# Kernel tuning notes

Measured on AMD Instinct MI355X. Metric: run time of the kernel, lower is better.

The kernel has to match this reference:

```python
import jax, jax.numpy as jnp
import numpy as np

ALPHA = jnp.full((8,), 0.25, dtype=jnp.float32)  # per-class focal alpha
GAMMA = 2.0
TEMP = 0.07
CIRC_TARGET = 1.0
CIRC_WEIGHT = 0.1
MIN_AGREE = 0.6
W_FOCAL, W_CONTRAST, W_CONSENSUS = 1.0, 0.5, 0.3


def setup_inputs() -> dict:
    key = jax.random.key(0)
    k1, k2, k3, k4, k5 = jax.random.split(key, 5)
    return {
        "logits": jax.random.normal(k1, (32, 8, 256, 256), dtype=jnp.float32),
        "target": jax.random.randint(k2, (32, 256, 256), 0, 8, dtype=jnp.int32),
        "features": jax.random.normal(k3, (1024, 512), dtype=jnp.float32),
        "masks": jax.random.uniform(k4, (32, 3, 256, 256), dtype=jnp.float32),
        "method_preds": jax.random.uniform(k5, (3, 32, 256, 256), dtype=jnp.float32),
    }


def focal_loss(logits, target):
    B, C, H, W = logits.shape
    x = logits.transpose(0, 2, 3, 1).reshape(-1, C)  # [BHW, C]
    t = target.reshape(-1)
    logp = jax.nn.log_softmax(x, axis=-1)
    ce = -jnp.take_along_axis(logp, t[:, None], axis=1)[:, 0]
    p = jnp.exp(-ce)
    focal_w = ALPHA[t] * (1.0 - p) ** GAMMA
    return jnp.mean(focal_w * ce)


def contrastive_loss(features):
    Bf = features.shape[0]
    f = features / jnp.linalg.norm(features, axis=1, keepdims=True)
    sim = (f @ f.T) / TEMP  # [Bf, Bf]
    # default labels = arange(Bf//2) tiled twice -> each sample has exactly one
    # positive: its paired view at index (i + Bf//2) % Bf
    pos_idx = (jnp.arange(Bf) + Bf // 2) % Bf
    pos = sim[jnp.arange(Bf), pos_idx]
    diag = jnp.eye(Bf, dtype=bool)
    # logits row i = {positive_i} U negatives_i = all j != i (single positive case)
    masked = jnp.where(diag, -1e30, sim)
    lse = jax.nn.logsumexp(masked, axis=1)
    return jnp.mean(lse - pos)  # CE with target = the (only) positive


def circularity_loss(masks):
    m = masks[:, 0]  # [B, H, W] core channel
    B = m.shape[0]
    area = jnp.sum(m, axis=(1, 2))
    ex = jnp.sum(jnp.abs(m[:, 1:, :] - m[:, :-1, :]), axis=(1, 2))
    ey = jnp.sum(jnp.abs(m[:, :, 1:] - m[:, :, :-1]), axis=(1, 2))
    per = ex + ey
    circ = 4.0 * np.pi * area / jnp.maximum(per, 1e-12) ** 2
    li = jnp.where((area > 0) & (per > 0), (circ - CIRC_TARGET) ** 2, 0.0)
    return CIRC_WEIGHT * jnp.sum(li) / B


def consensus_loss(method_preds):
    K = method_preds.shape[0]
    total, n = 0.0, 0
    for i in range(K):  # K=3 methods -> 3 pairs (fixed, small)
        for j in range(i + 1, K):
            pi, pj = method_preds[i], method_preds[j]
            inter = jnp.sum(pi * pj)
            union = jnp.sum(pi + pj - pi * pj)
            iou = inter / (union + 1e-6)
            total = total + jax.nn.relu(MIN_AGREE - iou)
            n += 1
    return total / n


def reference(logits, target, features, masks, method_preds):
    return (W_FOCAL * focal_loss(logits, target)
            + W_CONTRAST * contrastive_loss(features)
            + circularity_loss(masks)
            + W_CONSENSUS * consensus_loss(method_preds))
```

## Files before the change

kernel.cpp:

```cpp
#include <hip/hip_runtime.h>
#include <math.h>

#define WS_FOCALP 0
#define WS_CONSP  2048
#define WS_AREAP  14336
#define WS_EXP_   14848
#define WS_EYP_   15360
#define WS_POS    15872
#define WS_PART   16896
#define WS_HI_B   393216
#define WS_LO_B   1441792

typedef __attribute__((ext_vector_type(8))) short bf16x8;
typedef __attribute__((ext_vector_type(4))) float f32x4;

__device__ inline float wave_reduce(float v) {
#pragma unroll
  for (int m = 32; m >= 1; m >>= 1) v += __shfl_xor(v, m);
  return v;
}

__device__ inline unsigned short bf16_rne(float x) {
  union { float f; unsigned u; } v; v.f = x;
  unsigned r = v.u + 0x7FFF + ((v.u >> 16) & 1);
  return (unsigned short)(r >> 16);
}
__device__ inline float bf16_f(unsigned short h) {
  union { unsigned u; float f; } v; v.u = ((unsigned)h) << 16; return v.f;
}

__device__ inline float focal_px(float v0, float v1, float v2, float v3,
                                 float v4, float v5, float v6, float v7, int tt) {
  float mx = fmaxf(fmaxf(fmaxf(v0, v1), fmaxf(v2, v3)),
                   fmaxf(fmaxf(v4, v5), fmaxf(v6, v7)));
  float se = __expf(v0 - mx) + __expf(v1 - mx) + __expf(v2 - mx) + __expf(v3 - mx) +
             __expf(v4 - mx) + __expf(v5 - mx) + __expf(v6 - mx) + __expf(v7 - mx);
  float xt = v0;
  xt = (tt == 1) ? v1 : xt;
  xt = (tt == 2) ? v2 : xt;
  xt = (tt == 3) ? v3 : xt;
  xt = (tt == 4) ? v4 : xt;
  xt = (tt == 5) ? v5 : xt;
  xt = (tt == 6) ? v6 : xt;
  xt = (tt == 7) ? v7 : xt;
  float lp = (xt - mx) - __logf(se);
  float p = __expf(lp);
  float om = 1.0f - p;
  return 0.25f * om * om * (-lp);
}

__global__ __launch_bounds__(256) void prep_kernel(const float* __restrict__ feat,
                                                   float* __restrict__ ws) {
  const int tid = threadIdx.x;
  const int lane = tid & 63;
  const int wid = tid >> 6;
  int row = blockIdx.x * 4 + wid;
  const float4* f4 = (const float4*)feat;
  float4 u = f4[row * 128 + lane];
  float4 w = f4[row * 128 + 64 + lane];
  float s = u.x * u.x + u.y * u.y + u.z * u.z + u.w * u.w +
            w.x * w.x + w.y * w.y + w.z * w.z + w.w * w.w;
  s = wave_reduce(s);
  float scale = 3.7796447300922719f / sqrtf(s);
  float g[8] = {u.x * scale, u.y * scale, u.z * scale, u.w * scale,
                w.x * scale, w.y * scale, w.z * scale, w.w * scale};
  unsigned short h[8];
  unsigned short l[8];
#pragma unroll
  for (int i = 0; i < 8; i++) {
    h[i] = bf16_rne(g[i]);
    l[i] = bf16_rne(g[i] - bf16_f(h[i]));
  }
  char* hb = (char*)ws + WS_HI_B + row * 1024;
  char* lb = (char*)ws + WS_LO_B + row * 1024;
  *(ushort4*)(hb + lane * 8) = make_ushort4(h[0], h[1], h[2], h[3]);
  *(ushort4*)(hb + 512 + lane * 8) = make_ushort4(h[4], h[5], h[6], h[7]);
  *(ushort4*)(lb + lane * 8) = make_ushort4(l[0], l[1], l[2], l[3]);
  *(ushort4*)(lb + 512 + lane * 8) = make_ushort4(l[4], l[5], l[6], l[7]);
}

__global__ __launch_bounds__(256) void fused_kernel(
    const float* __restrict__ logits, const int* __restrict__ target,
    const float* __restrict__ masks, const float* __restrict__ preds,
    float* __restrict__ ws) {
  __shared__ __align__(16) char lds[49152];
  const int bid = blockIdx.x;
  const int tid = threadIdx.x;
  const int lane = tid & 63;
  const int wid = tid >> 6;

  if (bid < 512) {
    const int wr = wid >> 1, wc = wid & 1;
    const int rt = bid >> 4, ct = bid & 15;
    const int rb = rt * 32, cb = ct * 64;
    const int hi8 = lane >> 4;
    const int l15 = lane & 15;
    const int lr_a = wr * 16 + l15;
    const int rb0 = wc * 32 + l15;
    const int rb1 = rb0 + 16;

    f32x4 acc0 = {0.f, 0.f, 0.f, 0.f};
    f32x4 acc1 = {0.f, 0.f, 0.f, 0.f};

    auto stage = [&](int ch) {
      const char* srcA = (const char*)ws + (ch < 8 ? WS_HI_B : WS_LO_B);
      const char* srcB = (const char*)ws + ((ch >> 2) == 1 ? WS_LO_B : WS_HI_B);
      int koff = (ch & 3) * 256;
      char* dst = lds + (ch & 1) * 24576;
#pragma unroll
      for (int rr = 0; rr < 6; rr++) {
        int idx = rr * 256 + tid;
        const char* g;
        if (rr < 2) {
          int row = idx >> 4, sl = idx & 15;
          g = srcA + (rb + row) * 1024 + koff + ((sl ^ (row & 7)) << 4);
        } else {
          int i2 = idx - 512;
          int row = i2 >> 4, sl = i2 & 15;
          g = srcB + (cb + row) * 1024 + koff + ((sl ^ (row & 7)) << 4);
        }
        __builtin_amdgcn_global_load_lds(
            (const __attribute__((address_space(1))) unsigned int*)g,
            (__attribute__((address_space(3))) unsigned int*)(dst + idx * 16),
            16, 0, 0);
      }
    };

    auto compute = [&](int buf) {
      const char* bp = lds + buf * 24576;
#pragma unroll
      for (int j = 0; j < 4; j++) {
        int sa = (j * 4 + hi8) ^ (lr_a & 7);
        bf16x8 a = *(const bf16x8*)(bp + lr_a * 256 + sa * 16);
        int sb0 = (j * 4 + hi8) ^ (rb0 & 7);
        bf16x8 b0 = *(const bf16x8*)(bp + 8192 + rb0 * 256 + sb0 * 16);
        int sb1 = (j * 4 + hi8) ^ (rb1 & 7);
        bf16x8 b1 = *(const bf16x8*)(bp + 8192 + rb1 * 256 + sb1 * 16);
        acc0 = __builtin_amdgcn_mfma_f32_16x16x32_bf16(a, b0, acc0, 0, 0, 0);
        acc1 = __builtin_amdgcn_mfma_f32_16x16x32_bf16(a, b1, acc1, 0, 0, 0);
      }
    };

    stage(0);
    __syncthreads();
#pragma unroll 1
    for (int ch = 0; ch < 12; ch++) {
      if (ch + 1 < 12) stage(ch + 1);
      compute(ch & 1);
      __syncthreads();
    }

    int c0 = cb + wc * 32 + l15;
    int c1 = c0 + 16;
    float2* part = (float2*)(ws + WS_PART);
#pragma unroll
    for (int q = 0; q < 4; q++) {
      int r = rb + wr * 16 + hi8 * 4 + q;
      float v0 = acc0[q], v1 = acc1[q];
      int pc = (r + 512) & 1023;
      if (c0 == pc) ws[WS_POS + r] = v0;
      if (c1 == pc) ws[WS_POS + r] = v1;
      if (c0 == r) v0 = -1e30f;
      if (c1 == r) v1 = -1e30f;
      float m = fmaxf(v0, v1);
      float s = __expf(v0 - m) + __expf(v1 - m);
#pragma unroll
      for (int d = 1; d < 16; d <<= 1) {
        float mo = __shfl_xor(m, d), so = __shfl_xor(s, d);
        float nm = fmaxf(m, mo);
        s = s * __expf(m - nm) + so * __expf(mo - nm);
        m = nm;
      }
      if (l15 == 0) part[r * 32 + ct * 2 + wc] = make_float2(m, s);
    }
    return;
  }

  float* red = (float*)lds;
  const int bid2 = bid - 512;

  if (bid2 < 2048) {
    int t = bid2 * 256 + tid;
    int p4 = t * 4;
    int b = p4 >> 16;
    int hw = p4 & 65535;
    const float* lb = logits + (b << 19) + hw;
    float4 x0 = *(const float4*)(lb + (0 << 16));
    float4 x1 = *(const float4*)(lb + (1 << 16));
    float4 x2 = *(const float4*)(lb + (2 << 16));
    float4 x3 = *(const float4*)(lb + (3 << 16));
    float4 x4 = *(const float4*)(lb + (4 << 16));
    float4 x5 = *(const float4*)(lb + (5 << 16));
    float4 x6 = *(const float4*)(lb + (6 << 16));
    float4 x7 = *(const float4*)(lb + (7 << 16));
    int4 tg = *(const int4*)(target + p4);
    float acc = 0.0f;
    acc += focal_px(x0.x, x1.x, x2.x, x3.x, x4.x, x5.x, x6.x, x7.x, tg.x);
    acc += focal_px(x0.y, x1.y, x2.y, x3.y, x4.y, x5.y, x6.y, x7.y, tg.y);
    acc += focal_px(x0.z, x1.z, x2.z, x3.z, x4.z, x5.z, x6.z, x7.z, tg.z);
    acc += focal_px(x0.w, x1.w, x2.w, x3.w, x4.w, x5.w, x6.w, x7.w, tg.w);
    float v = wave_reduce(acc);
    if (lane == 0) red[wid] = v;
    __syncthreads();
    if (tid == 0) ws[WS_FOCALP + bid2] = red[0] + red[1] + red[2] + red[3];

  } else if (bid2 < 2560) {
    int bi = bid2 - 2048;
    int img = bi >> 4;
    int part = bi & 15;
    const float* mS = masks + img * 3 * 65536;
    const float4* m4 = (const float4*)mS;
    float a = 0.0f, ex = 0.0f, ey = 0.0f;
#pragma unroll
    for (int i = 0; i < 4; i++) {
      int v = tid + 256 * i;
      int rl = v >> 6;
      int c4 = v & 63;
      int row = part * 16 + rl;
      float4 val = m4[row * 64 + c4];
      a += val.x + val.y + val.z + val.w;
      ey += fabsf(val.y - val.x) + fabsf(val.z - val.y) + fabsf(val.w - val.z);
      if (c4 > 0) ey += fabsf(val.x - mS[row * 256 + c4 * 4 - 1]);
      if (row > 0) {
        float4 u = m4[(row - 1) * 64 + c4];
        ex += fabsf(val.x - u.x) + fabsf(val.y - u.y) +
              fabsf(val.z - u.z) + fabsf(val.w - u.w);
      }
    }
    float ra = wave_reduce(a);
    float rx = wave_reduce(ex);
    float ry = wave_reduce(ey);
    if (lane == 0) {
      red[wid + 0] = ra; red[wid + 4] = rx; red[wid + 8] = ry;
    }
    __syncthreads();
    if (tid == 0) {
      ws[WS_AREAP + bi] = red[0] + red[1] + red[2] + red[3];
      ws[WS_EXP_ + bi] = red[4] + red[5] + red[6] + red[7];
      ws[WS_EYP_ + bi] = red[8] + red[9] + red[10] + red[11];
    }

  } else {
    int b = bid2 - 2560;
    int t = b * 256 + tid;
    const float4* q = (const float4*)preds;
    float4 a0 = q[t];
    float4 a1 = q[t + 524288];
    float4 a2 = q[t + 1048576];
    float s0 = a0.x + a0.y + a0.z + a0.w;
    float s1 = a1.x + a1.y + a1.z + a1.w;
    float s2 = a2.x + a2.y + a2.z + a2.w;
    float p01 = a0.x * a1.x + a0.y * a1.y + a0.z * a1.z + a0.w * a1.w;
    float p02 = a0.x * a2.x + a0.y * a2.y + a0.z * a2.z + a0.w * a2.w;
    float p12 = a1.x * a2.x + a1.y * a2.y + a1.z * a2.z + a1.w * a2.w;
    float r0 = wave_reduce(s0);
    float r1 = wave_reduce(s1);
    float r2 = wave_reduce(s2);
    float r3 = wave_reduce(p01);
    float r4 = wave_reduce(p02);
    float r5 = wave_reduce(p12);
    if (lane == 0) {
      red[wid + 0] = r0; red[wid + 4] = r1; red[wid + 8] = r2;
      red[wid + 12] = r3; red[wid + 16] = r4; red[wid + 20] = r5;
    }
    __syncthreads();
    if (tid == 0) {
#pragma unroll
      for (int k = 0; k < 6; k++)
        ws[WS_CONSP + k * 2048 + b] =
            red[k * 4] + red[k * 4 + 1] + red[k * 4 + 2] + red[k * 4 + 3];
    }
  }
}

__device__ inline float block_reduce_1024(float v, float* red) {
  int tid = threadIdx.x;
  v = wave_reduce(v);
  __syncthreads();
  if ((tid & 63) == 0) red[tid >> 6] = v;
  __syncthreads();
  float t = 0.0f;
  if (tid == 0) {
#pragma unroll
    for (int i = 0; i < 16; i++) t += red[i];
  }
  return t;
}

__global__ __launch_bounds__(1024) void final_kernel(float* __restrict__ ws,
                                                     float* __restrict__ out) {
  __shared__ float red[16];
  __shared__ float li_s[32];
  int r = threadIdx.x;

  const float2* part = (const float2*)(ws + WS_PART);
  float M = -1e30f, S = 0.0f;
#pragma unroll
  for (int ctl = 0; ctl < 32; ctl++) {
    float2 p = part[r * 32 + ctl];
    float nm = fmaxf(M, p.x);
    S = S * __expf(M - nm) + p.y * __expf(p.x - nm);
    M = nm;
  }
  float lse = M + __logf(S);
  float contr_sum = block_reduce_1024(lse - ws[WS_POS + r], red);

  float focal_sum =
      block_reduce_1024(ws[WS_FOCALP + r] + ws[WS_FOCALP + r + 1024], red);

  float cons[6];
#pragma unroll
  for (int k = 0; k < 6; k++) {
    const float* p = ws + WS_CONSP + k * 2048;
    cons[k] = block_reduce_1024(p[r] + p[r + 1024], red);
  }

  float li = 0.0f;
  if (r < 512) {
    float a = ws[WS_AREAP + r];
    float ex = ws[WS_EXP_ + r];
    float ey = ws[WS_EYP_ + r];
#pragma unroll
    for (int d = 1; d < 16; d <<= 1) {
      a += __shfl_xor(a, d);
      ex += __shfl_xor(ex, d);
      ey += __shfl_xor(ey, d);
    }
    if ((r & 15) == 0) {
      float per = ex + ey;
      float dd = fmaxf(per, 1e-12f);
      float c = 12.566370614359172f * a / (dd * dd);
      li = (a > 0.0f && per > 0.0f) ? (c - 1.0f) * (c - 1.0f) : 0.0f;
      li_s[r >> 4] = li;
    }
  }
  __syncthreads();

  if (r == 0) {
    float circ = 0.0f;
#pragma unroll
    for (int i = 0; i < 32; i++) circ += li_s[i];
    circ = 0.1f * circ / 32.0f;

    float contr = contr_sum / 1024.0f;
    float focal = focal_sum / 2097152.0f;

    float S0 = cons[0], S1 = cons[1], S2 = cons[2];
    float P01 = cons[3], P02 = cons[4], P12 = cons[5];
    float co = 0.0f;
    co += fmaxf(0.6f - P01 / (S0 + S1 - P01 + 1e-6f), 0.0f);
    co += fmaxf(0.6f - P02 / (S0 + S2 - P02 + 1e-6f), 0.0f);
    co += fmaxf(0.6f - P12 / (S1 + S2 - P12 + 1e-6f), 0.0f);
    co *= (1.0f / 3.0f);

    out[0] = focal + 0.5f * contr + circ + 0.3f * co;
  }
}

extern "C" void kernel_launch(void* const* d_in, const int* in_sizes, int n_in,
                              void* d_out, int out_size, void* d_ws, size_t ws_size,
                              hipStream_t stream) {
  const float* logits = (const float*)d_in[0];
  const int* target = (const int*)d_in[1];
  const float* feat = (const float*)d_in[2];
  const float* masks = (const float*)d_in[3];
  const float* preds = (const float*)d_in[4];
  float* ws = (float*)d_ws;
  float* out = (float*)d_out;

  prep_kernel<<<256, 256, 0, stream>>>(feat, ws);
  fused_kernel<<<5120, 256, 0, stream>>>(logits, target, masks, preds, ws);
  final_kernel<<<1, 1024, 0, stream>>>(ws, out);
}
```

Measured before the change: 50.18 us.

## Replace LDS-staged GEMM with larger register-tiled direct-global MFMA tiles

The similarity GEMM blocks now compute 64x128 tiles instead of 32x64, which cuts the GEMM block count from 512 to 128. Operands are read straight from global memory into registers, dropping the LDS double-buffering and its barriers. The per-block LDS allocation shrinks from 48KB to a tiny reduction buffer, which should raise occupancy for the co-resident focal, circularity and consensus blocks. The trade is less data reuse per load, uncoalesced 16-byte strided global reads that depend on L2, and higher register pressure from 8 accumulators.

```diff
diff --git a/kernel.cpp b/kernel.cpp
--- a/kernel.cpp
+++ b/kernel.cpp
@@ -83,101 +83,87 @@
     const float* __restrict__ logits, const int* __restrict__ target,
     const float* __restrict__ masks, const float* __restrict__ preds,
     float* __restrict__ ws) {
-  __shared__ __align__(16) char lds[49152];
+  __shared__ float red[32];
   const int bid = blockIdx.x;
   const int tid = threadIdx.x;
   const int lane = tid & 63;
   const int wid = tid >> 6;
 
-  if (bid < 512) {
+  if (bid < 128) {
+    const int rt = bid >> 3, ct = bid & 7;
     const int wr = wid >> 1, wc = wid & 1;
-    const int rt = bid >> 4, ct = bid & 15;
-    const int rb = rt * 32, cb = ct * 64;
+    const int l15 = lane & 15;
     const int hi8 = lane >> 4;
-    const int l15 = lane & 15;
-    const int lr_a = wr * 16 + l15;
-    const int rb0 = wc * 32 + l15;
-    const int rb1 = rb0 + 16;
-
-    f32x4 acc0 = {0.f, 0.f, 0.f, 0.f};
-    f32x4 acc1 = {0.f, 0.f, 0.f, 0.f};
-
-    auto stage = [&](int ch) {
-      const char* srcA = (const char*)ws + (ch < 8 ? WS_HI_B : WS_LO_B);
-      const char* srcB = (const char*)ws + ((ch >> 2) == 1 ? WS_LO_B : WS_HI_B);
-      int koff = (ch & 3) * 256;
-      char* dst = lds + (ch & 1) * 24576;
-#pragma unroll
-      for (int rr = 0; rr < 6; rr++) {
-        int idx = rr * 256 + tid;
-        const char* g;
-        if (rr < 2) {
-          int row = idx >> 4, sl = idx & 15;
-          g = srcA + (rb + row) * 1024 + koff + ((sl ^ (row & 7)) << 4);
-        } else {
-          int i2 = idx - 512;
-          int row = i2 >> 4, sl = i2 & 15;
-          g = srcB + (cb + row) * 1024 + koff + ((sl ^ (row & 7)) << 4);
+    const char* HI = (const char*)ws + WS_HI_B;
+    const char* LO = (const char*)ws + WS_LO_B;
+    const int ar = rt * 64 + wr * 32 + l15;
+    const int bc = ct * 128 + wc * 64 + l15;
+    const int kb16 = hi8 * 16;
+
+    f32x4 acc[2][4];
+#pragma unroll
+    for (int r = 0; r < 2; r++)
+#pragma unroll
+      for (int c = 0; c < 4; c++) acc[r][c] = (f32x4){0.f, 0.f, 0.f, 0.f};
+
+#pragma unroll 2
+    for (int kb = 0; kb < 16; kb++) {
+      int ko = kb * 64 + kb16;
+      bf16x8 ah[2], al[2], bh[4], bl[4];
+#pragma unroll
+      for (int r = 0; r < 2; r++) {
+        ah[r] = *(const bf16x8*)(HI + (ar + r * 16) * 1024 + ko);
+        al[r] = *(const bf16x8*)(LO + (ar + r * 16) * 1024 + ko);
+      }
+#pragma unroll
+      for (int c = 0; c < 4; c++) {
+        bh[c] = *(const bf16x8*)(HI + (bc + c * 16) * 1024 + ko);
+        bl[c] = *(const bf16x8*)(LO + (bc + c * 16) * 1024 + ko);
+      }
+#pragma unroll
+      for (int r = 0; r < 2; r++)
+#pragma unroll
+        for (int c = 0; c < 4; c++) {
+          acc[r][c] = __builtin_amdgcn_mfma_f32_16x16x32_bf16(ah[r], bh[c], acc[r][c], 0, 0, 0);
+          acc[r][c] = __builtin_amdgcn_mfma_f32_16x16x32_bf16(ah[r], bl[c], acc[r][c], 0, 0, 0);
+          acc[r][c] = __builtin_amdgcn_mfma_f32_16x16x32_bf16(al[r], bh[c], acc[r][c], 0, 0, 0);
         }
-        __builtin_amdgcn_global_load_lds(
-            (const __attribute__((address_space(1))) unsigned int*)g,
-            (__attribute__((address_space(3))) unsigned int*)(dst + idx * 16),
-            16, 0, 0);
+    }
+
+    float2* part = (float2*)(ws + WS_PART);
+#pragma unroll
+    for (int r = 0; r < 2; r++)
+#pragma unroll
+      for (int q = 0; q < 4; q++) {
+        int row = rt * 64 + wr * 32 + r * 16 + hi8 * 4 + q;
+        int pc = (row + 512) & 1023;
+        float m = -3e38f;
+        float v[4];
+#pragma unroll
+        for (int c = 0; c < 4; c++) {
+          int col = ct * 128 + wc * 64 + c * 16 + l15;
+          float x = acc[r][c][q];
+          if (col == pc) ws[WS_POS + row] = x;
+          if (col == row) x = -1e30f;
+          v[c] = x;
+          m = fmaxf(m, x);
+        }
+        float s = 0.f;
+#pragma unroll
+        for (int c = 0; c < 4; c++) s += __expf(v[c] - m);
+#pragma unroll
+        for (int d = 1; d < 16; d <<= 1) {
+          float mo = __shfl_xor(m, d), so = __shfl_xor(s, d);
+          float nm = fmaxf(m, mo);
+          s = s * __expf(m - nm) + so * __expf(mo - nm);
+          m = nm;
+        }
+        if (l15 == 0) part[row * 16 + ct * 2 + wc] = make_float2(m, s);
       }
-    };
-
-    auto compute = [&](int buf) {
-      const char* bp = lds + buf * 24576;
-#pragma unroll
-      for (int j = 0; j < 4; j++) {
-        int sa = (j * 4 + hi8) ^ (lr_a & 7);
-        bf16x8 a = *(const bf16x8*)(bp + lr_a * 256 + sa * 16);
-        int sb0 = (j * 4 + hi8) ^ (rb0 & 7);
-        bf16x8 b0 = *(const bf16x8*)(bp + 8192 + rb0 * 256 + sb0 * 16);
-        int sb1 = (j * 4 + hi8) ^ (rb1 & 7);
-        bf16x8 b1 = *(const bf16x8*)(bp + 8192 + rb1 * 256 + sb1 * 16);
-        acc0 = __builtin_amdgcn_mfma_f32_16x16x32_bf16(a, b0, acc0, 0, 0, 0);
-        acc1 = __builtin_amdgcn_mfma_f32_16x16x32_bf16(a, b1, acc1, 0, 0, 0);
-      }
-    };
-
-    stage(0);
-    __syncthreads();
-#pragma unroll 1
-    for (int ch = 0; ch < 12; ch++) {
-      if (ch + 1 < 12) stage(ch + 1);
-      compute(ch & 1);
-      __syncthreads();
-    }
-
-    int c0 = cb + wc * 32 + l15;
-    int c1 = c0 + 16;
-    float2* part = (float2*)(ws + WS_PART);
-#pragma unroll
-    for (int q = 0; q < 4; q++) {
-      int r = rb + wr * 16 + hi8 * 4 + q;
-      float v0 = acc0[q], v1 = acc1[q];
-      int pc = (r + 512) & 1023;
-      if (c0 == pc) ws[WS_POS + r] = v0;
-      if (c1 == pc) ws[WS_POS + r] = v1;
-      if (c0 == r) v0 = -1e30f;
-      if (c1 == r) v1 = -1e30f;
-      float m = fmaxf(v0, v1);
-      float s = __expf(v0 - m) + __expf(v1 - m);
-#pragma unroll
-      for (int d = 1; d < 16; d <<= 1) {
-        float mo = __shfl_xor(m, d), so = __shfl_xor(s, d);
-        float nm = fmaxf(m, mo);
-        s = s * __expf(m - nm) + so * __expf(mo - nm);
-        m = nm;
-      }
-      if (l15 == 0) part[r * 32 + ct * 2 + wc] = make_float2(m, s);
-    }
     return;
   }
 
-  float* red = (float*)lds;
-  const int bid2 = bid - 512;
+  const int bid2 = bid - 128;
 
   if (bid2 < 2048) {
     int t = bid2 * 256 + tid;
@@ -296,8 +282,8 @@
   const float2* part = (const float2*)(ws + WS_PART);
   float M = -1e30f, S = 0.0f;
 #pragma unroll
-  for (int ctl = 0; ctl < 32; ctl++) {
-    float2 p = part[r * 32 + ctl];
+  for (int ctl = 0; ctl < 16; ctl++) {
+    float2 p = part[r * 16 + ctl];
     float nm = fmaxf(M, p.x);
     S = S * __expf(M - nm) + p.y * __expf(p.x - nm);
     M = nm;
@@ -369,6 +355,6 @@
   float* out = (float*)d_out;
 
   prep_kernel<<<256, 256, 0, stream>>>(feat, ws);
-  fused_kernel<<<5120, 256, 0, stream>>>(logits, target, masks, preds, ws);
+  fused_kernel<<<4736, 256, 0, stream>>>(logits, target, masks, preds, ws);
   final_kernel<<<1, 1024, 0, stream>>>(ws, out);
 }
```

After: 54.36 us. 1.08x slower.
